# Performance work log

Hardware: AMD Instinct MI355X
Metric: run time of the kernel (lower is better)

The kernel has to match this reference:

```python
import jax, jax.numpy as jnp
from jax import lax
import numpy as np

NEG = -1e10  # matches the -10000000000.0 boundary in the torch code


def _nw_forward(theta, A):
    """Needleman-Wunsch DP with softmax (logsumexp) smoothed max.

    V[i, j] = theta[i-1, j-1] + LSE(A + V[i-1, j], V[i-1, j-1], A + V[i, j-1])
    with V[0, 0] = 0 and V[i, 0] = V[0, j] = -1e10 otherwise.
    Vectorized over anti-diagonals (wavefront): diag d holds V[i, d-i].
    """
    N, M = theta.shape
    i_idx = jnp.arange(N + 1)

    # diag d=0: only V[0,0]=0 is on it; diag d=1: V[0,1]=V[1,0]=NEG
    d0 = jnp.full((N + 1,), NEG, dtype=theta.dtype).at[0].set(0.0)
    d1 = jnp.full((N + 1,), NEG, dtype=theta.dtype)

    def step(carry, d):
        pprev, prev = carry  # diagonals d-2 and d-1, indexed by i
        j = d - i_idx
        valid = (i_idx >= 1) & (j >= 1) & (j <= M)
        pad = jnp.full((1,), NEG, dtype=theta.dtype)
        up = jnp.concatenate([pad, prev[:-1]])     # V[i-1, j]   (diag d-1, idx i-1)
        diag = jnp.concatenate([pad, pprev[:-1]])  # V[i-1, j-1] (diag d-2, idx i-1)
        left = prev                                # V[i, j-1]   (diag d-1, idx i)
        ic = jnp.clip(i_idx - 1, 0, N - 1)
        jc = jnp.clip(j - 1, 0, M - 1)
        th = jnp.where(valid, theta[ic, jc], 0.0)
        # candidates in original order (x, m, y)
        cand = jnp.stack([A + up, diag, A + left], axis=-1)  # (N+1, 3)
        v = th + jax.nn.logsumexp(cand, axis=-1)
        new = jnp.where(valid, v, NEG)
        return (prev, new), None

    ds = jnp.arange(2, N + M + 1)
    (_, last), _ = lax.scan(step, (d0, d1), ds)
    return last[N]  # V[N, M] lives on diagonal d = N + M at index i = N


def setup_inputs() -> dict:
    key = jax.random.key(0)
    N, M = 2048, 2048
    theta = jax.random.normal(key, (N, M), dtype=jnp.float32)
    A = jnp.asarray(-4.0, dtype=jnp.float32)  # scalar gap penalty
    return {"theta": theta, "A": A}


def reference(theta, A):
    return _nw_forward(theta, A)
```

## Files before the change

### kernel.cpp

```cpp
#include <hip/hip_runtime.h>


constexpr int NDP = 2048;
constexpr int MDP = 2048;
constexpr int G    = 16;
constexpr int RPW  = 128;
constexpr int BATCH = 32;
constexpr int NB    = 68;
constexpr int DTOT  = NDP + MDP;
constexpr int DVB   = 4160;
constexpr float LOG2E = 1.44269504088896340736f;
constexpr float LN2   = 0.69314718055994530942f;

__device__ __forceinline__ float neginf() { return __int_as_float(0xff800000); }

__global__ __launch_bounds__(64)
void nw_pipe(const float* __restrict__ theta, const float* __restrict__ Aptr,
             float* __restrict__ out, float* __restrict__ vbBase,
             int* __restrict__ flags)
{
  const int wg   = blockIdx.x;
  const int lane = threadIdx.x;

  const float A  = Aptr[0];
  const float eA = __builtin_exp2f(A * LOG2E);

  const int S   = wg * RPW + 2;
  const int rA0 = wg * RPW + 2 * lane;
  const int rB0 = rA0 + 1;
  const float* thA_p = theta + (size_t)rA0 * MDP;
  const float* thB_p = theta + (size_t)rB0 * MDP;
  const int endA = rA0 + 1 + MDP;
  const int endB = endA + 1;

  float* vbMine = vbBase + (size_t)wg * DVB;
  const float* vbProd = vbBase + (size_t)(wg - 1) * DVB;
  int* flagProd = flags + (wg - 1) * 16;
  int* flagMine = flags + wg * 16;
  const int eMaxProd = (wg > 0) ? (wg * RPW + MDP) : -1;

  float WA1 = 0.f, WA2 = 0.f, WB1 = 0.f, WB2 = 0.f;
  float bu = 0.f, bd = (wg == 0) ? 1.f : 0.f;
  float oaccF = 0.f;
  bool  init  = (wg == 0);
  float corner = 0.f;
  float vbReg = neginf();

  float tba[4][8], tbb[4][8];
#pragma unroll
  for (int u = 0; u < 4; ++u)
#pragma unroll
    for (int k = 0; k < 8; ++k) {
      int d  = S + 8 * u + k;
      int cA = min(max(d - (rA0 + 1) - 1, 0), MDP - 1);
      int cB = min(max(d - (rB0 + 1) - 1, 0), MDP - 1);
      tba[u][k] = thA_p[cA];
      tbb[u][k] = thB_p[cB];
    }

  if (wg > 0) {
    const int E0 = S - 1;
    const int need = min(E0 + 31, eMaxProd);
    while (__hip_atomic_load(flagProd, __ATOMIC_ACQUIRE, __HIP_MEMORY_SCOPE_AGENT) < need)
      __builtin_amdgcn_s_sleep(2);
    int e = E0 + (lane & 31);
    vbReg = (e <= eMaxProd) ? vbProd[e] : neginf();
    float m = vbReg;
#pragma unroll
    for (int sh = 1; sh < 64; sh <<= 1) m = fmaxf(m, __shfl_xor(m, sh, 64));
    if (m > -1e30f) { oaccF = m; init = true; }
    bu = __builtin_exp2f(fminf(__shfl(vbReg, 0, 64) - oaccF, 120.f));
  }

  for (int b = 0; b < NB; ++b) {
    const int dBase = S + BATCH * b;
#pragma unroll
    for (int u = 0; u < 4; ++u) {
#pragma unroll
      for (int k = 0; k < 8; ++k) {
        const int d = dBase + 8 * u + k;
        float upA = __shfl_up(WB1, 1, 64);
        float dgA = __shfl_up(WB2, 1, 64);
        if (lane == 0) { upA = bu; dgA = bd; }
        const float tA = __builtin_exp2f(tba[u][k] * LOG2E);
        const float tB = __builtin_exp2f(tbb[u][k] * LOG2E);
        float nA = tA * (eA * (upA + WA1) + dgA);
        float nB = tB * (eA * (WA1 + WB1) + WA2);
        nA = (d <= endA) ? nA : 0.f;
        nB = (d <= endB) ? nB : 0.f;
        WA2 = WA1; WA1 = nA; WB2 = WB1; WB1 = nB;
        if (lane == 63) {
          float vlog = __builtin_log2f(WB1) + oaccF;
          vbMine[d] = vlog;
          if (d == DTOT) corner = vlog;
        }
        bd = bu;
        if (!(u == 3 && k == 7)) {
          float v = __shfl(vbReg, 8 * u + k + 1, 64);
          bu = __builtin_exp2f(fminf(v - oaccF, 120.f));
        }
      }
      {
        float m = fmaxf(fmaxf(WA1, WB1), fmaxf(WA2, WB2));
        m = fmaxf(m, fmaxf(bu, bd));
#pragma unroll
        for (int sh = 1; sh < 64; sh <<= 1) m = fmaxf(m, __shfl_xor(m, sh, 64));
        int e = 0;
        if (m > 0.f) e = (int)((__float_as_uint(m) >> 23) & 0xFFu) - 126;
        if (e != 0) {
          WA1 = ldexpf(WA1, -e); WA2 = ldexpf(WA2, -e);
          WB1 = ldexpf(WB1, -e); WB2 = ldexpf(WB2, -e);
          bu  = ldexpf(bu,  -e); bd  = ldexpf(bd,  -e);
          oaccF += (float)e;
        }
      }
      if (b + 1 < NB) {
#pragma unroll
        for (int k = 0; k < 8; ++k) {
          int d  = dBase + BATCH + 8 * u + k;
          int cA = min(max(d - (rA0 + 1) - 1, 0), MDP - 1);
          int cB = min(max(d - (rB0 + 1) - 1, 0), MDP - 1);
          tba[u][k] = thA_p[cA];
          tbb[u][k] = thB_p[cB];
        }
      }
    }
    if (wg < G - 1 && lane == 63)
      __hip_atomic_store(flagMine, dBase + BATCH - 1, __ATOMIC_RELEASE, __HIP_MEMORY_SCOPE_AGENT);
    if (b + 1 < NB && wg > 0) {
      const int E0 = S - 1 + BATCH * (b + 1);
      if (E0 <= eMaxProd) {
        const int need = min(E0 + 31, eMaxProd);
        while (__hip_atomic_load(flagProd, __ATOMIC_ACQUIRE, __HIP_MEMORY_SCOPE_AGENT) < need)
          __builtin_amdgcn_s_sleep(2);
        int e = E0 + (lane & 31);
        vbReg = (e <= eMaxProd) ? vbProd[e] : neginf();
      } else vbReg = neginf();
      if (!init) {
        float m = vbReg;
#pragma unroll
        for (int sh = 1; sh < 64; sh <<= 1) m = fmaxf(m, __shfl_xor(m, sh, 64));
        if (m > -1e30f) { oaccF = m; init = true; }
      }
      bu = __builtin_exp2f(fminf(__shfl(vbReg, 0, 64) - oaccF, 120.f));
    }
  }

  if (wg == G - 1 && lane == 63) out[0] = corner * LN2;
}

constexpr int NTH = 512;
constexpr int RPT = 4;
constexpr int NWAVE = NTH / 64;

__global__ __launch_bounds__(NTH)
void nw_single(const float* __restrict__ th, const float* __restrict__ Aptr,
               float* __restrict__ out)
{
  const int tid  = threadIdx.x;
  const int lane = tid & 63;
  const int wid  = tid >> 6;
  __shared__ float handW[2][NTH];
  __shared__ float wmax[2][NWAVE];
  const float A  = Aptr[0];
  const float eA = __builtin_exp2f(A * LOG2E);
  const int i_base = tid * RPT + 1;
  float W10=0.f,W11=0.f,W12=0.f,W13=0.f,W20=0.f,W21=0.f,W22=0.f,W23=0.f;
  float nb1 = 0.f, nb2 = (tid == 0) ? 1.f : 0.f;
  int oacc = 0;
  const float* thb = th + (size_t)(i_base - 1) * MDP;
  auto loadTh = [&](int d) -> float4 {
    float4 r;
    int c0 = min(max(d - i_base - 1, 0), MDP - 1);
    int c1 = min(max(d - i_base - 2, 0), MDP - 1);
    int c2 = min(max(d - i_base - 3, 0), MDP - 1);
    int c3 = min(max(d - i_base - 4, 0), MDP - 1);
    r.x = thb[c0]; r.y = thb[(size_t)MDP + c1];
    r.z = thb[(size_t)2 * MDP + c2]; r.w = thb[(size_t)3 * MDP + c3];
    return r;
  };
  float4 thA = loadTh(2), thB = loadTh(3);
  for (int d = 2; d <= DTOT; ++d) {
    float4 thC = loadTh(d + 2);
    float n0 = __builtin_exp2f(thA.x*LOG2E)*(eA*(nb1+W10)+nb2);
    float n1 = __builtin_exp2f(thA.y*LOG2E)*(eA*(W10+W11)+W20);
    float n2 = __builtin_exp2f(thA.z*LOG2E)*(eA*(W11+W12)+W21);
    float n3 = __builtin_exp2f(thA.w*LOG2E)*(eA*(W12+W13)+W22);
    W20=W10;W21=W11;W22=W12;W23=W13;
    int cb = d - i_base - 1;
    W10 = ((unsigned)(cb)     < (unsigned)MDP) ? n0 : 0.f;
    W11 = ((unsigned)(cb - 1) < (unsigned)MDP) ? n1 : 0.f;
    W12 = ((unsigned)(cb - 2) < (unsigned)MDP) ? n2 : 0.f;
    W13 = ((unsigned)(cb - 3) < (unsigned)MDP) ? n3 : 0.f;
    const int buf = d & 1;
    const bool rs = ((d & 1) == 0);
    const int wbuf = (d >> 1) & 1;
    if (rs) {
      float m = fmaxf(fmaxf(W10,W11),fmaxf(W12,W13));
#pragma unroll
      for (int sh = 1; sh < 64; sh <<= 1) m = fmaxf(m, __shfl_xor(m, sh, 64));
      if (lane == 0) wmax[wbuf][wid] = m;
    }
    handW[buf][tid] = W13;
    __syncthreads();
    nb2 = nb1;
    nb1 = (tid == 0) ? 0.f : handW[buf][tid - 1];
    if (rs) {
      float bm = wmax[wbuf][0];
#pragma unroll
      for (int w = 1; w < NWAVE; ++w) bm = fmaxf(bm, wmax[wbuf][w]);
      int e = 0;
      if (bm > 0.f) e = (int)((__float_as_uint(bm) >> 23) & 0xFFu) - 126;
      if (e != 0) {
        W10=ldexpf(W10,-e);W11=ldexpf(W11,-e);W12=ldexpf(W12,-e);W13=ldexpf(W13,-e);
        W20=ldexpf(W20,-e);W21=ldexpf(W21,-e);W22=ldexpf(W22,-e);W23=ldexpf(W23,-e);
        nb1=ldexpf(nb1,-e);nb2=ldexpf(nb2,-e);
        oacc += e;
      }
    }
    thA = thB; thB = thC;
  }
  if (tid == NTH - 1) out[0] = logf(W13) + (float)oacc * LN2;
}

extern "C" void kernel_launch(void* const* d_in, const int* in_sizes, int n_in,
                              void* d_out, int out_size, void* d_ws, size_t ws_size,
                              hipStream_t stream)
{
  const float* theta = (const float*)d_in[0];
  const float* A     = (const float*)d_in[1];
  float* out = (float*)d_out;

  const size_t need = (size_t)G * DVB * sizeof(float) + G * 16 * sizeof(int);
  if (ws_size >= need) {
    float* vb  = (float*)d_ws;
    int* flags = (int*)((char*)d_ws + (size_t)G * DVB * sizeof(float));
    hipLaunchKernelGGL(nw_pipe, dim3(G), dim3(64), 0, stream, theta, A, out, vb, flags);
  } else {
    hipLaunchKernelGGL(nw_single, dim3(1), dim3(NTH), 0, stream, theta, A, out);
  }
}
```

Baseline: 1.152 ms.

## Use inline-asm sc0 sc1 loads/stores for inter-workgroup handoff and drop a shuffle

Replaces the acquire/release atomics and plain global accesses used for the cross-workgroup boundary handoff with inline-asm global loads and stores carrying sc0 sc1 cache bits. The flag store is preceded by an explicit vmcnt(0) wait, and the spin sleep is shortened. This aims to cut the cache-flush and invalidate overhead that full acquire/release fences add on the critical wavefront handoff path. It also removes one shuffle per step by reusing the previous step's up value as the diagonal input, and enlarges the per-workgroup buffer stride. The trade-off is that correctness now depends on hand-written memory ordering instead of the compiler's fences.

```diff
diff --git a/kernel.cpp b/kernel.cpp
--- a/kernel.cpp
+++ b/kernel.cpp
@@ -8,11 +8,31 @@
 constexpr int BATCH = 32;
 constexpr int NB    = 68;
 constexpr int DTOT  = NDP + MDP;
-constexpr int DVB   = 4160;
+constexpr int DVB   = 4224;
 constexpr float LOG2E = 1.44269504088896340736f;
 constexpr float LN2   = 0.69314718055994530942f;
 
 __device__ __forceinline__ float neginf() { return __int_as_float(0xff800000); }
+
+__device__ __forceinline__ void ic_store(float* p, float v) {
+  asm volatile("global_store_dword %0, %1, off sc0 sc1" :: "v"(p), "v"(v));
+}
+__device__ __forceinline__ void ic_store_flag(int* p, int v) {
+  asm volatile("s_waitcnt vmcnt(0)\n\tglobal_store_dword %0, %1, off sc0 sc1"
+               :: "v"(p), "v"(v));
+}
+__device__ __forceinline__ float ic_load(const float* p) {
+  float r;
+  asm volatile("global_load_dword %0, %1, off sc0 sc1\n\ts_waitcnt vmcnt(0)"
+               : "=v"(r) : "v"(p));
+  return r;
+}
+__device__ __forceinline__ int ic_load_flag(const int* p) {
+  int r;
+  asm volatile("global_load_dword %0, %1, off sc0 sc1\n\ts_waitcnt vmcnt(0)"
+               : "=v"(r) : "v"(p) : "memory");
+  return r;
+}
 
 __global__ __launch_bounds__(64)
 void nw_pipe(const float* __restrict__ theta, const float* __restrict__ Aptr,
@@ -39,7 +59,8 @@
   int* flagMine = flags + wg * 16;
   const int eMaxProd = (wg > 0) ? (wg * RPW + MDP) : -1;
 
-  float WA1 = 0.f, WA2 = 0.f, WB1 = 0.f, WB2 = 0.f;
+  float WA1 = 0.f, WA2 = 0.f, WB1 = 0.f;
+  float upPrev = 0.f;
   float bu = 0.f, bd = (wg == 0) ? 1.f : 0.f;
   float oaccF = 0.f;
   bool  init  = (wg == 0);
@@ -61,10 +82,11 @@
   if (wg > 0) {
     const int E0 = S - 1;
     const int need = min(E0 + 31, eMaxProd);
-    while (__hip_atomic_load(flagProd, __ATOMIC_ACQUIRE, __HIP_MEMORY_SCOPE_AGENT) < need)
-      __builtin_amdgcn_s_sleep(2);
-    int e = E0 + (lane & 31);
-    vbReg = (e <= eMaxProd) ? vbProd[e] : neginf();
+    while (ic_load_flag(flagProd) < need) __builtin_amdgcn_s_sleep(1);
+    int e  = E0 + (lane & 31);
+    int eL = min(max(e, 0), eMaxProd);
+    float v0 = ic_load(vbProd + eL);
+    vbReg = (e <= eMaxProd) ? v0 : neginf();
     float m = vbReg;
 #pragma unroll
     for (int sh = 1; sh < 64; sh <<= 1) m = fmaxf(m, __shfl_xor(m, sh, 64));
@@ -80,18 +102,18 @@
       for (int k = 0; k < 8; ++k) {
         const int d = dBase + 8 * u + k;
         float upA = __shfl_up(WB1, 1, 64);
-        float dgA = __shfl_up(WB2, 1, 64);
-        if (lane == 0) { upA = bu; dgA = bd; }
+        if (lane == 0) upA = bu;
+        float dgA = (lane == 0) ? bd : upPrev;
         const float tA = __builtin_exp2f(tba[u][k] * LOG2E);
         const float tB = __builtin_exp2f(tbb[u][k] * LOG2E);
         float nA = tA * (eA * (upA + WA1) + dgA);
         float nB = tB * (eA * (WA1 + WB1) + WA2);
         nA = (d <= endA) ? nA : 0.f;
         nB = (d <= endB) ? nB : 0.f;
-        WA2 = WA1; WA1 = nA; WB2 = WB1; WB1 = nB;
+        WA2 = WA1; WA1 = nA; WB1 = nB; upPrev = upA;
         if (lane == 63) {
           float vlog = __builtin_log2f(WB1) + oaccF;
-          vbMine[d] = vlog;
+          ic_store(vbMine + d, vlog);
           if (d == DTOT) corner = vlog;
         }
         bd = bu;
@@ -101,16 +123,16 @@
         }
       }
       {
-        float m = fmaxf(fmaxf(WA1, WB1), fmaxf(WA2, WB2));
+        float m = fmaxf(fmaxf(WA1, WB1), fmaxf(WA2, upPrev));
         m = fmaxf(m, fmaxf(bu, bd));
 #pragma unroll
         for (int sh = 1; sh < 64; sh <<= 1) m = fmaxf(m, __shfl_xor(m, sh, 64));
         int e = 0;
         if (m > 0.f) e = (int)((__float_as_uint(m) >> 23) & 0xFFu) - 126;
         if (e != 0) {
-          WA1 = ldexpf(WA1, -e); WA2 = ldexpf(WA2, -e);
-          WB1 = ldexpf(WB1, -e); WB2 = ldexpf(WB2, -e);
-          bu  = ldexpf(bu,  -e); bd  = ldexpf(bd,  -e);
+          WA1 = ldexpf(WA1, -e); WA2 = ldexpf(WA2, -e); WB1 = ldexpf(WB1, -e);
+          upPrev = ldexpf(upPrev, -e);
+          bu = ldexpf(bu, -e); bd = ldexpf(bd, -e);
           oaccF += (float)e;
         }
       }
@@ -126,16 +148,19 @@
       }
     }
     if (wg < G - 1 && lane == 63)
-      __hip_atomic_store(flagMine, dBase + BATCH - 1, __ATOMIC_RELEASE, __HIP_MEMORY_SCOPE_AGENT);
+      ic_store_flag(flagMine, dBase + BATCH - 1);
     if (b + 1 < NB && wg > 0) {
       const int E0 = S - 1 + BATCH * (b + 1);
       if (E0 <= eMaxProd) {
         const int need = min(E0 + 31, eMaxProd);
-        while (__hip_atomic_load(flagProd, __ATOMIC_ACQUIRE, __HIP_MEMORY_SCOPE_AGENT) < need)
-          __builtin_amdgcn_s_sleep(2);
-        int e = E0 + (lane & 31);
-        vbReg = (e <= eMaxProd) ? vbProd[e] : neginf();
-      } else vbReg = neginf();
+        while (ic_load_flag(flagProd) < need) __builtin_amdgcn_s_sleep(1);
+        int e  = E0 + (lane & 31);
+        int eL = min(max(e, 0), eMaxProd);
+        float v0 = ic_load(vbProd + eL);
+        vbReg = (e <= eMaxProd) ? v0 : neginf();
+      } else {
+        vbReg = neginf();
+      }
       if (!init) {
         float m = vbReg;
 #pragma unroll
```

Result: no change. 1.154 ms (+0.2%).
